# Kernel tuning notes

Hardware: AMD Instinct MI355X
Metric: run time of the kernel (lower is better)

## Reference

```python
import jax, jax.numpy as jnp
import numpy as np

TOKENS = 32768
HIDDEN = 2048
N_EXPERTS = 128
TOP_K = 8
NORM_TOPK_PROB = True


def setup_inputs() -> dict:
    key = jax.random.key(0)
    k1, k2 = jax.random.split(key)
    hidden_states = jax.random.normal(k1, (TOKENS, HIDDEN), dtype=jnp.float32)
    # router weight [num_experts, hidden_dim]; small init like a trained gate
    weight = jax.random.normal(k2, (N_EXPERTS, HIDDEN), dtype=jnp.float32) * 0.02
    return {"hidden_states": hidden_states, "weight": weight}


def reference(hidden_states, weight):
    # flatten tokens (already [T, H])
    x = hidden_states.reshape(-1, HIDDEN)
    # router logits: [T, E]
    logits = jnp.einsum("th,eh->te", x, weight)
    # softmax in float32 (matches dtype=torch.float)
    probs = jax.nn.softmax(logits.astype(jnp.float32), axis=-1)
    # top-k over experts
    top_val, top_idx = jax.lax.top_k(probs, TOP_K)  # [T, K], [T, K]
    if NORM_TOPK_PROB:
        top_val = top_val / jnp.sum(top_val, axis=-1, keepdims=True)
    top_val = top_val.astype(probs.dtype)
    # scatter renormalized weights into dense [T, E] score tensor
    rows = jnp.arange(x.shape[0])[:, None]  # [T, 1]
    scores = jnp.zeros_like(probs).at[rows, top_idx].set(top_val)
    return scores, top_idx
```

## Files before the change

### kernel.cpp

```cpp
#include <hip/hip_runtime.h>
#include <hip/hip_bf16.h>

#define NT   32768
#define NH   2048
#define NE   128
#define TOPK 8
#define BT   32
#define BND    6.0e-4f
#define TWO_B  (2.0f * BND)

#define WS_W_OFF   64
#define WS_REC_U32 262160

typedef __attribute__((ext_vector_type(8))) short bf16x8;
typedef __attribute__((ext_vector_type(4))) float f32x4;

static __device__ __forceinline__ unsigned short f2bf(float f) {
    __hip_bfloat16 h = __float2bfloat16(f);
    return *reinterpret_cast<unsigned short*>(&h);
}

__global__ __launch_bounds__(256) void prep_w_kernel(
    const float* __restrict__ W, unsigned short* __restrict__ Wt)
{
    int g = blockIdx.x * 256 + threadIdx.x;
    int lane = g & 63;
    int te   = (g >> 6) & 7;
    int s    = (g >> 9) & 1;
    int k32  = g >> 10;
    int row  = te * 16 + (lane & 15);
    int kb   = k32 * 32 + (lane >> 4) * 8;
    const float* src = W + (size_t)row * NH + kb;
    float4 f0 = *(const float4*)src;
    float4 f1 = *(const float4*)(src + 4);
    float f[8] = {f0.x, f0.y, f0.z, f0.w, f1.x, f1.y, f1.z, f1.w};
    bf16x8 o;
    #pragma unroll
    for (int e = 0; e < 8; ++e) {
        unsigned short h = f2bf(f[e]);
        if (s == 0) o[e] = (short)h;
        else {
            float fh = __builtin_bit_cast(float, ((unsigned int)h) << 16);
            o[e] = (short)f2bf(f[e] - fh);
        }
    }
    *(bf16x8*)(Wt + (size_t)g * 8) = o;
}

__global__ __launch_bounds__(256, 3) void router_gemm_kernel(
    const float* __restrict__ X, const unsigned short* __restrict__ Wt,
    float* __restrict__ out, unsigned int* __restrict__ ws)
{
    __shared__ float ps[2][BT * 132];

    const int tid  = threadIdx.x;
    const int lane = tid & 63;
    const int w    = tid >> 6;
    const int l15  = lane & 15, lhi = lane >> 4;
    const int t0   = blockIdx.x * BT;

    f32x4 acc[2][8];
    #pragma unroll
    for (int i = 0; i < 2; ++i)
        #pragma unroll
        for (int te = 0; te < 8; ++te) acc[i][te] = (f32x4){0.f, 0.f, 0.f, 0.f};

    const float* x0 = X + (size_t)(t0 + l15) * NH + lhi * 8;
    const float* x1 = X + (size_t)(t0 + 16 + l15) * NH + lhi * 8;
    const int kbase = w * 512;

    #pragma unroll 2
    for (int kk = 0; kk < 16; ++kk) {
        const int k = kbase + kk * 32;
        bf16x8 ah[2], al[2];
        #pragma unroll
        for (int i = 0; i < 2; ++i) {
            const float* xp = (i ? x1 : x0) + k;
            float4 fa = *(const float4*)xp;
            float4 fb = *(const float4*)(xp + 4);
            float f[8] = {fa.x, fa.y, fa.z, fa.w, fb.x, fb.y, fb.z, fb.w};
            #pragma unroll
            for (int e = 0; e < 8; ++e) {
                unsigned short h = f2bf(f[e]);
                ah[i][e] = (short)h;
                float fh = __builtin_bit_cast(float, ((unsigned int)h) << 16);
                al[i][e] = (short)f2bf(f[e] - fh);
            }
        }
        const unsigned short* wb = Wt + (size_t)(w * 16 + kk) * 8192;
        #pragma unroll
        for (int te = 0; te < 8; ++te) {
            bf16x8 bh = *(const bf16x8*)(wb + te * 512 + lane * 8);
            bf16x8 bl = *(const bf16x8*)(wb + 4096 + te * 512 + lane * 8);
            acc[0][te] = __builtin_amdgcn_mfma_f32_16x16x32_bf16(ah[0], bh, acc[0][te], 0, 0, 0);
            acc[1][te] = __builtin_amdgcn_mfma_f32_16x16x32_bf16(ah[1], bh, acc[1][te], 0, 0, 0);
            acc[0][te] = __builtin_amdgcn_mfma_f32_16x16x32_bf16(al[0], bh, acc[0][te], 0, 0, 0);
            acc[1][te] = __builtin_amdgcn_mfma_f32_16x16x32_bf16(al[1], bh, acc[1][te], 0, 0, 0);
            acc[0][te] = __builtin_amdgcn_mfma_f32_16x16x32_bf16(ah[0], bl, acc[0][te], 0, 0, 0);
            acc[1][te] = __builtin_amdgcn_mfma_f32_16x16x32_bf16(ah[1], bl, acc[1][te], 0, 0, 0);
        }
    }

    if (w < 2) {
        #pragma unroll
        for (int i = 0; i < 2; ++i)
            #pragma unroll
            for (int te = 0; te < 8; ++te)
                #pragma unroll
                for (int q = 0; q < 4; ++q)
                    ps[w][(i * 16 + lhi * 4 + q) * 132 + te * 16 + l15] = acc[i][te][q];
    }
    __syncthreads();
    if (w >= 2) {
        #pragma unroll
        for (int i = 0; i < 2; ++i)
            #pragma unroll
            for (int te = 0; te < 8; ++te)
                #pragma unroll
                for (int q = 0; q < 4; ++q) {
                    int o = (i * 16 + lhi * 4 + q) * 132 + te * 16 + l15;
                    ps[w - 2][o] += acc[i][te][q];
                }
    }
    __syncthreads();
    #pragma unroll
    for (int q = 0; q < 4; ++q) {
        int idx = tid + q * 256;
        int row = idx >> 5, c4 = idx & 31;
        int o = row * 132 + c4 * 4;
        float4 a = *(float4*)&ps[0][o];
        float4 b = *(float4*)&ps[1][o];
        a.x += b.x; a.y += b.y; a.z += b.z; a.w += b.w;
        *(float4*)&ps[0][o] = a;
    }
    float* scoreBase = out + (size_t)t0 * NE;
    #pragma unroll
    for (int q = 0; q < 4; ++q) {
        int i = tid + q * 256;
        *(float4*)(scoreBase + (size_t)i * 4) = make_float4(0.f, 0.f, 0.f, 0.f);
    }
    __syncthreads();

    if (tid < BT) {
        const float* row = &ps[0][tid * 132];
        float tv[13]; int ti[13];
        #pragma unroll
        for (int k = 0; k < 13; ++k) { tv[k] = -3.0e38f; ti[k] = 0; }
        for (int e = 0; e < NE; ++e) {
            float v = row[e];
            if (v > tv[12]) {
                float cv = v; int ci = e;
                #pragma unroll
                for (int s = 0; s < 13; ++s) {
                    if (cv > tv[s]) {
                        float t1 = tv[s]; int t2 = ti[s];
                        tv[s] = cv; ti[s] = ci; cv = t1; ci = t2;
                    }
                }
            }
        }
        bool flag = false;
        #pragma unroll
        for (int k = 0; k < 8; ++k) flag |= (tv[k] - tv[k + 1] < TWO_B);

        float pv[8]; float ksum = 0.f;
        #pragma unroll
        for (int k = 0; k < 8; ++k) { pv[k] = expf(tv[k] - tv[0]); ksum += pv[k]; }
        const int tg = t0 + tid;
        float* srow = out + (size_t)tg * NE;
        float* irow = out + (size_t)NT * NE + (size_t)tg * TOPK;
        #pragma unroll
        for (int k = 0; k < 8; ++k) {
            srow[ti[k]] = pv[k] / ksum;
            irow[k] = (float)ti[k];
        }

        if (flag) {
            unsigned int cnt;
            unsigned int idw[4] = {0u, 0u, 0u, 0u};
            float thr = tv[7] - TWO_B;
            if (tv[12] >= thr) {
                cnt = 0xFFu;
            } else {
                cnt = 0;
                #pragma unroll
                for (int k = 0; k < 13; ++k) {
                    if (k < 8 || tv[k] >= thr) {
                        idw[cnt >> 2] |= ((unsigned int)ti[k]) << ((cnt & 3) * 8);
                        ++cnt;
                    }
                }
            }
            unsigned int slot = atomicAdd(ws, 1u);
            unsigned int* rec = ws + WS_REC_U32 + slot * 8;
            rec[0] = (unsigned int)tg;
            rec[1] = cnt;
            rec[2] = idw[0]; rec[3] = idw[1]; rec[4] = idw[2]; rec[5] = idw[3];
        }
    }
}

__global__ __launch_bounds__(256) void finalize_kernel(
    const float* __restrict__ X, const float* __restrict__ W,
    float* __restrict__ out, const unsigned int* __restrict__ ws)
{
    __shared__ float  xs[2048];
    __shared__ double cv[128];
    __shared__ int    cid[128];
    __shared__ float  ovals[8];
    __shared__ int    oidx[8];

    const int tid = threadIdx.x;
    const int lane = tid & 63, w = tid >> 6;
    const unsigned int n = ws[0];

    for (unsigned int rI = blockIdx.x; rI < n; rI += gridDim.x) {
        const unsigned int* rec = ws + WS_REC_U32 + rI * 8;
        const int tg = (int)rec[0];
        const unsigned int cnt = rec[1];
        const unsigned char* ids = (const unsigned char*)(rec + 2);
        const int nc = (cnt == 0xFFu) ? NE : (int)cnt;

        #pragma unroll
        for (int q = 0; q < 2; ++q) {
            int i = tid + q * 256;
            *(float4*)(xs + i * 4) = *(const float4*)(X + (size_t)tg * NH + i * 4);
        }
        __syncthreads();

        for (int c = w; c < nc; c += 4) {
            int e = (cnt == 0xFFu) ? c : (int)ids[c];
            const float* wrow = W + (size_t)e * NH;
            double s = 0.0;
            #pragma unroll
            for (int m = 0; m < 8; ++m) {
                float4 wv = *(const float4*)(wrow + m * 256 + lane * 4);
                float4 xv = *(const float4*)(xs + m * 256 + lane * 4);
                s = fma((double)xv.x, (double)wv.x, s);
                s = fma((double)xv.y, (double)wv.y, s);
                s = fma((double)xv.z, (double)wv.z, s);
                s = fma((double)xv.w, (double)wv.w, s);
            }
            #pragma unroll
            for (int off = 32; off >= 1; off >>= 1) s += __shfl_xor(s, off);
            if (lane == 0) { cv[c] = s; cid[c] = e; }
        }
        __syncthreads();

        if (tid == 0) {
            double lv[8];
            #pragma unroll
            for (int k = 0; k < 8; ++k) {
                double best = -1.0e300; int bi = 1 << 30, bc = 0;
                for (int c = 0; c < nc; ++c) {
                    double v = cv[c]; int e = cid[c];
                    if (v > best || (v == best && e < bi)) { best = v; bi = e; bc = c; }
                }
                lv[k] = best; oidx[k] = bi; cv[bc] = -1.0e301;
            }
            double m = lv[0], sum = 0.0, p[8];
            #pragma unroll
            for (int k = 0; k < 8; ++k) { p[k] = exp(lv[k] - m); sum += p[k]; }
            #pragma unroll
            for (int k = 0; k < 8; ++k) ovals[k] = (float)(p[k] / sum);
        }
        __syncthreads();

        float* srow = out + (size_t)tg * NE;
        if (tid < NE) {
            float val = 0.f;
            #pragma unroll
            for (int k = 0; k < 8; ++k) if (oidx[k] == tid) val = ovals[k];
            srow[tid] = val;
        }
        if (tid < TOPK) out[(size_t)NT * NE + (size_t)tg * TOPK + tid] = (float)oidx[tid];
        __syncthreads();
    }
}

extern "C" void kernel_launch(void* const* d_in, const int* in_sizes, int n_in,
                              void* d_out, int out_size, void* d_ws, size_t ws_size,
                              hipStream_t stream) {
    const float* X = (const float*)d_in[0];
    const float* W = (const float*)d_in[1];
    float* out = (float*)d_out;
    unsigned char* wsb = (unsigned char*)d_ws;
    unsigned short* Wt = (unsigned short*)(wsb + WS_W_OFF);

    hipMemsetAsync(d_ws, 0, 64, stream);
    prep_w_kernel<<<256, 256, 0, stream>>>(W, Wt);
    router_gemm_kernel<<<NT / BT, 256, 0, stream>>>(X, Wt, out, (unsigned int*)d_ws);
    finalize_kernel<<<1024, 256, 0, stream>>>(X, W, out, (const unsigned int*)d_ws);
}
```

Measured before the change: 196.8 us.

## Double-buffer W fragments, bit-trick bf16 split, move top-k to separate kernel

The GEMM loop now prefetches the next k-step's W fragments into registers (double buffering) while the current MFMAs run. It also replaces the library bf16 conversion with integer round-half-up bit tricks, and lowers the occupancy hint from 3 to 2. The top-k selection, which previously ran on only 32 threads per block, moves to a separate kernel with one token per thread that reads logits written to the output buffer. The trade-off is an extra global round trip for the logits and another kernel launch, plus higher register pressure. The new rounding (add 0x8000) differs from round-to-nearest-even only in tie cases.

```diff
diff --git a/kernel.cpp b/kernel.cpp
--- a/kernel.cpp
+++ b/kernel.cpp
@@ -14,6 +14,7 @@
 
 typedef __attribute__((ext_vector_type(8))) short bf16x8;
 typedef __attribute__((ext_vector_type(4))) float f32x4;
+typedef __attribute__((ext_vector_type(4))) unsigned int u32x4;
 
 static __device__ __forceinline__ unsigned short f2bf(float f) {
     __hip_bfloat16 h = __float2bfloat16(f);
@@ -47,9 +48,9 @@
     *(bf16x8*)(Wt + (size_t)g * 8) = o;
 }
 
-__global__ __launch_bounds__(256, 3) void router_gemm_kernel(
+__global__ __launch_bounds__(256, 2) void router_gemm_kernel(
     const float* __restrict__ X, const unsigned short* __restrict__ Wt,
-    float* __restrict__ out, unsigned int* __restrict__ ws)
+    float* __restrict__ outLg)
 {
     __shared__ float ps[2][BT * 132];
 
@@ -65,40 +66,68 @@
         #pragma unroll
         for (int te = 0; te < 8; ++te) acc[i][te] = (f32x4){0.f, 0.f, 0.f, 0.f};
 
-    const float* x0 = X + (size_t)(t0 + l15) * NH + lhi * 8;
-    const float* x1 = X + (size_t)(t0 + 16 + l15) * NH + lhi * 8;
-    const int kbase = w * 512;
-
-    #pragma unroll 2
-    for (int kk = 0; kk < 16; ++kk) {
-        const int k = kbase + kk * 32;
+    const float* x0 = X + (size_t)(t0 + l15) * NH + w * 512 + lhi * 8;
+    const float* x1 = x0 + 16 * NH;
+    const unsigned short* wbase = Wt + (size_t)(w * 16) * 8192 + lane * 8;
+
+    bf16x8 b0[8][2], b1[8][2];
+
+    #define LOADB(arr, kk) do {                                                \
+        const unsigned short* wb_ = wbase + (size_t)(kk) * 8192;               \
+        _Pragma("unroll")                                                      \
+        for (int te = 0; te < 8; ++te) {                                       \
+            arr[te][0] = *(const bf16x8*)(wb_ + te * 512);                     \
+            arr[te][1] = *(const bf16x8*)(wb_ + 4096 + te * 512);              \
+        }                                                                      \
+    } while (0)
+
+    #define SPLITA(kk, ah, al) do {                                            \
+        _Pragma("unroll")                                                      \
+        for (int i = 0; i < 2; ++i) {                                          \
+            const float* xp = (i ? x1 : x0) + (kk) * 32;                       \
+            float4 fa = *(const float4*)xp;                                    \
+            float4 fb = *(const float4*)(xp + 4);                              \
+            float ff[8] = {fa.x, fa.y, fa.z, fa.w, fb.x, fb.y, fb.z, fb.w};    \
+            unsigned int hu[4], lu[4];                                         \
+            _Pragma("unroll")                                                  \
+            for (int p = 0; p < 4; ++p) {                                      \
+                unsigned int u0 = __builtin_bit_cast(unsigned int, ff[2*p]);   \
+                unsigned int u1 = __builtin_bit_cast(unsigned int, ff[2*p+1]); \
+                unsigned int r0 = u0 + 0x8000u, r1 = u1 + 0x8000u;             \
+                hu[p] = (r0 >> 16) | (r1 & 0xFFFF0000u);                       \
+                float h0 = __builtin_bit_cast(float, r0 & 0xFFFF0000u);        \
+                float h1 = __builtin_bit_cast(float, r1 & 0xFFFF0000u);        \
+                float e0 = ff[2*p] - h0, e1 = ff[2*p+1] - h1;                  \
+                unsigned int s0 = __builtin_bit_cast(unsigned int, e0) + 0x8000u; \
+                unsigned int s1 = __builtin_bit_cast(unsigned int, e1) + 0x8000u; \
+                lu[p] = (s0 >> 16) | (s1 & 0xFFFF0000u);                       \
+            }                                                                  \
+            ah[i] = __builtin_bit_cast(bf16x8, (u32x4){hu[0],hu[1],hu[2],hu[3]}); \
+            al[i] = __builtin_bit_cast(bf16x8, (u32x4){lu[0],lu[1],lu[2],lu[3]}); \
+        }                                                                      \
+    } while (0)
+
+    #define DOMFMA(b, ah, al) do {                                             \
+        _Pragma("unroll")                                                      \
+        for (int te = 0; te < 8; ++te) {                                       \
+            acc[0][te] = __builtin_amdgcn_mfma_f32_16x16x32_bf16(ah[0], b[te][0], acc[0][te], 0, 0, 0); \
+            acc[1][te] = __builtin_amdgcn_mfma_f32_16x16x32_bf16(ah[1], b[te][0], acc[1][te], 0, 0, 0); \
+            acc[0][te] = __builtin_amdgcn_mfma_f32_16x16x32_bf16(al[0], b[te][0], acc[0][te], 0, 0, 0); \
+            acc[1][te] = __builtin_amdgcn_mfma_f32_16x16x32_bf16(al[1], b[te][0], acc[1][te], 0, 0, 0); \
+            acc[0][te] = __builtin_amdgcn_mfma_f32_16x16x32_bf16(ah[0], b[te][1], acc[0][te], 0, 0, 0); \
+            acc[1][te] = __builtin_amdgcn_mfma_f32_16x16x32_bf16(ah[1], b[te][1], acc[1][te], 0, 0, 0); \
+        }                                                                      \
+    } while (0)
+
+    LOADB(b0, 0);
+    for (int p = 0; p < 8; ++p) {
         bf16x8 ah[2], al[2];
-        #pragma unroll
-        for (int i = 0; i < 2; ++i) {
-            const float* xp = (i ? x1 : x0) + k;
-            float4 fa = *(const float4*)xp;
-            float4 fb = *(const float4*)(xp + 4);
-            float f[8] = {fa.x, fa.y, fa.z, fa.w, fb.x, fb.y, fb.z, fb.w};
-            #pragma unroll
-            for (int e = 0; e < 8; ++e) {
-                unsigned short h = f2bf(f[e]);
-                ah[i][e] = (short)h;
-                float fh = __builtin_bit_cast(float, ((unsigned int)h) << 16);
-                al[i][e] = (short)f2bf(f[e] - fh);
-            }
-        }
-        const unsigned short* wb = Wt + (size_t)(w * 16 + kk) * 8192;
-        #pragma unroll
-        for (int te = 0; te < 8; ++te) {
-            bf16x8 bh = *(const bf16x8*)(wb + te * 512 + lane * 8);
-            bf16x8 bl = *(const bf16x8*)(wb + 4096 + te * 512 + lane * 8);
-            acc[0][te] = __builtin_amdgcn_mfma_f32_16x16x32_bf16(ah[0], bh, acc[0][te], 0, 0, 0);
-            acc[1][te] = __builtin_amdgcn_mfma_f32_16x16x32_bf16(ah[1], bh, acc[1][te], 0, 0, 0);
-            acc[0][te] = __builtin_amdgcn_mfma_f32_16x16x32_bf16(al[0], bh, acc[0][te], 0, 0, 0);
-            acc[1][te] = __builtin_amdgcn_mfma_f32_16x16x32_bf16(al[1], bh, acc[1][te], 0, 0, 0);
-            acc[0][te] = __builtin_amdgcn_mfma_f32_16x16x32_bf16(ah[0], bl, acc[0][te], 0, 0, 0);
-            acc[1][te] = __builtin_amdgcn_mfma_f32_16x16x32_bf16(ah[1], bl, acc[1][te], 0, 0, 0);
-        }
+        LOADB(b1, 2 * p + 1);
+        SPLITA(2 * p, ah, al);
+        DOMFMA(b0, ah, al);
+        if (p < 7) LOADB(b0, 2 * p + 2);
+        SPLITA(2 * p + 1, ah, al);
+        DOMFMA(b1, ah, al);
     }
 
     if (w < 2) {
@@ -125,31 +154,35 @@
     __syncthreads();
     #pragma unroll
     for (int q = 0; q < 4; ++q) {
-        int idx = tid + q * 256;
-        int row = idx >> 5, c4 = idx & 31;
+        int i = tid + q * 256;
+        int row = i >> 5, c4 = i & 31;
         int o = row * 132 + c4 * 4;
         float4 a = *(float4*)&ps[0][o];
         float4 b = *(float4*)&ps[1][o];
         a.x += b.x; a.y += b.y; a.z += b.z; a.w += b.w;
-        *(float4*)&ps[0][o] = a;
-    }
-    float* scoreBase = out + (size_t)t0 * NE;
-    #pragma unroll
-    for (int q = 0; q < 4; ++q) {
-        int i = tid + q * 256;
-        *(float4*)(scoreBase + (size_t)i * 4) = make_float4(0.f, 0.f, 0.f, 0.f);
-    }
-    __syncthreads();
-
-    if (tid < BT) {
-        const float* row = &ps[0][tid * 132];
-        float tv[13]; int ti[13];
-        #pragma unroll
-        for (int k = 0; k < 13; ++k) { tv[k] = -3.0e38f; ti[k] = 0; }
-        for (int e = 0; e < NE; ++e) {
-            float v = row[e];
+        *(float4*)(outLg + (size_t)(t0 + row) * NE + c4 * 4) = a;
+    }
+}
+
+__global__ __launch_bounds__(64) void select_kernel(
+    float* __restrict__ out, unsigned int* __restrict__ ws)
+{
+    const int tg = blockIdx.x * 64 + threadIdx.x;
+    float* row = out + (size_t)tg * NE;
+
+    float tv[13]; int ti[13];
+    #pragma unroll
+    for (int k = 0; k < 13; ++k) { tv[k] = -3.0e38f; ti[k] = 0; }
+
+    #pragma unroll 4
+    for (int c = 0; c < 32; ++c) {
+        float4 v4 = *(const float4*)(row + c * 4);
+        float vs[4] = {v4.x, v4.y, v4.z, v4.w};
+        #pragma unroll
+        for (int j = 0; j < 4; ++j) {
+            float v = vs[j];
             if (v > tv[12]) {
-                float cv = v; int ci = e;
+                float cv = v; int ci = c * 4 + j;
                 #pragma unroll
                 for (int s = 0; s < 13; ++s) {
                     if (cv > tv[s]) {
@@ -159,44 +192,49 @@
                 }
             }
         }
-        bool flag = false;
-        #pragma unroll
-        for (int k = 0; k < 8; ++k) flag |= (tv[k] - tv[k + 1] < TWO_B);
-
-        float pv[8]; float ksum = 0.f;
-        #pragma unroll
-        for (int k = 0; k < 8; ++k) { pv[k] = expf(tv[k] - tv[0]); ksum += pv[k]; }
-        const int tg = t0 + tid;
-        float* srow = out + (size_t)tg * NE;
-        float* irow = out + (size_t)NT * NE + (size_t)tg * TOPK;
-        #pragma unroll
-        for (int k = 0; k < 8; ++k) {
-            srow[ti[k]] = pv[k] / ksum;
-            irow[k] = (float)ti[k];
-        }
-
-        if (flag) {
-            unsigned int cnt;
-            unsigned int idw[4] = {0u, 0u, 0u, 0u};
-            float thr = tv[7] - TWO_B;
-            if (tv[12] >= thr) {
-                cnt = 0xFFu;
-            } else {
-                cnt = 0;
-                #pragma unroll
-                for (int k = 0; k < 13; ++k) {
-                    if (k < 8 || tv[k] >= thr) {
-                        idw[cnt >> 2] |= ((unsigned int)ti[k]) << ((cnt & 3) * 8);
-                        ++cnt;
-                    }
+    }
+
+    bool flag = false;
+    #pragma unroll
+    for (int k = 0; k < 8; ++k) flag |= (tv[k] - tv[k + 1] < TWO_B);
+
+    float pv[8]; float ksum = 0.f;
+    #pragma unroll
+    for (int k = 0; k < 8; ++k) { pv[k] = expf(tv[k] - tv[0]); ksum += pv[k]; }
+
+    float4 z = make_float4(0.f, 0.f, 0.f, 0.f);
+    #pragma unroll
+    for (int c = 0; c < 32; ++c) *(float4*)(row + c * 4) = z;
+    #pragma unroll
+    for (int k = 0; k < 8; ++k) row[ti[k]] = pv[k] / ksum;
+
+    float* irow = out + (size_t)NT * NE + (size_t)tg * TOPK;
+    float4 i0 = make_float4((float)ti[0], (float)ti[1], (float)ti[2], (float)ti[3]);
+    float4 i1 = make_float4((float)ti[4], (float)ti[5], (float)ti[6], (float)ti[7]);
+    *(float4*)irow = i0;
+    *(float4*)(irow + 4) = i1;
+
+    if (flag) {
+        unsigned int cnt;
+        unsigned int idw[4] = {0u, 0u, 0u, 0u};
+        float thr = tv[7] - TWO_B;
+        if (tv[12] >= thr) {
+            cnt = 0xFFu;
+        } else {
+            cnt = 0;
+            #pragma unroll
+            for (int k = 0; k < 13; ++k) {
+                if (k < 8 || tv[k] >= thr) {
+                    idw[cnt >> 2] |= ((unsigned int)ti[k]) << ((cnt & 3) * 8);
+                    ++cnt;
                 }
             }
-            unsigned int slot = atomicAdd(ws, 1u);
-            unsigned int* rec = ws + WS_REC_U32 + slot * 8;
-            rec[0] = (unsigned int)tg;
-            rec[1] = cnt;
-            rec[2] = idw[0]; rec[3] = idw[1]; rec[4] = idw[2]; rec[5] = idw[3];
-        }
+        }
+        unsigned int slot = atomicAdd(ws, 1u);
+        unsigned int* rec = ws + WS_REC_U32 + slot * 8;
+        rec[0] = (unsigned int)tg;
+        rec[1] = cnt;
+        rec[2] = idw[0]; rec[3] = idw[1]; rec[4] = idw[2]; rec[5] = idw[3];
     }
 }
 
@@ -289,6 +327,7 @@
 
     hipMemsetAsync(d_ws, 0, 64, stream);
     prep_w_kernel<<<256, 256, 0, stream>>>(W, Wt);
-    router_gemm_kernel<<<NT / BT, 256, 0, stream>>>(X, Wt, out, (unsigned int*)d_ws);
+    router_gemm_kernel<<<NT / BT, 256, 0, stream>>>(X, Wt, out);
+    select_kernel<<<NT / 64, 64, 0, stream>>>(out, (unsigned int*)d_ws);
     finalize_kernel<<<1024, 256, 0, stream>>>(X, W, out, (const unsigned int*)d_ws);
 }
```

New measurement: 345.6 us. +75.6%, slower.

## Split router GEMM across 8 waves with prefetch and bit-trick bf16 split

Applied to the files above, without the earlier changes.

The router GEMM block grows from 256 to 512 threads. Each wave now handles one 16-token group over a quarter of K instead of both groups, which halves the accumulator registers per wave and raises occupancy. The loop prefetches the next X chunk into registers, and the fp32 to hi/lo bf16 split uses integer round-and-mask in place of conversion intrinsics. Partial sums are reduced through a transposed shared buffer over serialized passes with barriers. In exchange, each wave loads every W fragment without reusing it across two token groups, so W traffic per MFMA doubles.

```diff
diff --git a/kernel.cpp b/kernel.cpp
--- a/kernel.cpp
+++ b/kernel.cpp
@@ -5,7 +5,7 @@
 #define NH   2048
 #define NE   128
 #define TOPK 8
-#define BT   32
+#define BTOK 32
 #define BND    6.0e-4f
 #define TWO_B  (2.0f * BND)
 
@@ -14,6 +14,7 @@
 
 typedef __attribute__((ext_vector_type(8))) short bf16x8;
 typedef __attribute__((ext_vector_type(4))) float f32x4;
+typedef __attribute__((ext_vector_type(4))) unsigned int u32x4;
 
 static __device__ __forceinline__ unsigned short f2bf(float f) {
     __hip_bfloat16 h = __float2bfloat16(f);
@@ -47,107 +48,101 @@
     *(bf16x8*)(Wt + (size_t)g * 8) = o;
 }
 
-__global__ __launch_bounds__(256, 3) void router_gemm_kernel(
+__global__ __launch_bounds__(512, 4) void router_gemm_kernel(
     const float* __restrict__ X, const unsigned short* __restrict__ Wt,
     float* __restrict__ out, unsigned int* __restrict__ ws)
 {
-    __shared__ float ps[2][BT * 132];
+    __shared__ float ps[NE * 36];
 
     const int tid  = threadIdx.x;
     const int lane = tid & 63;
-    const int w    = tid >> 6;
+    const int wv   = tid >> 6;
+    const int g    = wv & 1;
+    const int h    = wv >> 1;
     const int l15  = lane & 15, lhi = lane >> 4;
-    const int t0   = blockIdx.x * BT;
-
-    f32x4 acc[2][8];
-    #pragma unroll
-    for (int i = 0; i < 2; ++i)
-        #pragma unroll
-        for (int te = 0; te < 8; ++te) acc[i][te] = (f32x4){0.f, 0.f, 0.f, 0.f};
-
-    const float* x0 = X + (size_t)(t0 + l15) * NH + lhi * 8;
-    const float* x1 = X + (size_t)(t0 + 16 + l15) * NH + lhi * 8;
-    const int kbase = w * 512;
-
-    #pragma unroll 2
+    const int t0   = blockIdx.x * BTOK;
+
+    f32x4 acc[8];
+    #pragma unroll
+    for (int te = 0; te < 8; ++te) acc[te] = (f32x4){0.f, 0.f, 0.f, 0.f};
+
+    const float* xrow = X + (size_t)(t0 + g * 16 + l15) * NH + h * 512 + lhi * 8;
+    const unsigned short* wq = Wt + (size_t)(h * 16) * 8192 + lane * 8;
+
+    float4 a0 = *(const float4*)(xrow);
+    float4 a1 = *(const float4*)(xrow + 4);
+
+    #pragma unroll
     for (int kk = 0; kk < 16; ++kk) {
-        const int k = kbase + kk * 32;
-        bf16x8 ah[2], al[2];
-        #pragma unroll
-        for (int i = 0; i < 2; ++i) {
-            const float* xp = (i ? x1 : x0) + k;
-            float4 fa = *(const float4*)xp;
-            float4 fb = *(const float4*)(xp + 4);
-            float f[8] = {fa.x, fa.y, fa.z, fa.w, fb.x, fb.y, fb.z, fb.w};
-            #pragma unroll
-            for (int e = 0; e < 8; ++e) {
-                unsigned short h = f2bf(f[e]);
-                ah[i][e] = (short)h;
-                float fh = __builtin_bit_cast(float, ((unsigned int)h) << 16);
-                al[i][e] = (short)f2bf(f[e] - fh);
-            }
-        }
-        const unsigned short* wb = Wt + (size_t)(w * 16 + kk) * 8192;
+        float4 n0, n1;
+        if (kk < 15) {
+            n0 = *(const float4*)(xrow + (kk + 1) * 32);
+            n1 = *(const float4*)(xrow + (kk + 1) * 32 + 4);
+        }
+        bf16x8 ah, al;
+        {
+            float ff[8] = {a0.x, a0.y, a0.z, a0.w, a1.x, a1.y, a1.z, a1.w};
+            unsigned int hu[4], lu[4];
+            #pragma unroll
+            for (int p = 0; p < 4; ++p) {
+                unsigned int u0 = __builtin_bit_cast(unsigned int, ff[2 * p]);
+                unsigned int u1 = __builtin_bit_cast(unsigned int, ff[2 * p + 1]);
+                unsigned int r0 = u0 + 0x8000u, r1 = u1 + 0x8000u;
+                hu[p] = (r0 >> 16) | (r1 & 0xFFFF0000u);
+                float h0 = __builtin_bit_cast(float, r0 & 0xFFFF0000u);
+                float h1 = __builtin_bit_cast(float, r1 & 0xFFFF0000u);
+                float e0 = ff[2 * p] - h0, e1 = ff[2 * p + 1] - h1;
+                unsigned int s0 = __builtin_bit_cast(unsigned int, e0);
+                unsigned int s1 = __builtin_bit_cast(unsigned int, e1);
+                lu[p] = (s0 >> 16) | (s1 & 0xFFFF0000u);
+            }
+            ah = __builtin_bit_cast(bf16x8, (u32x4){hu[0], hu[1], hu[2], hu[3]});
+            al = __builtin_bit_cast(bf16x8, (u32x4){lu[0], lu[1], lu[2], lu[3]});
+        }
+        const unsigned short* wb = wq + (size_t)kk * 8192;
         #pragma unroll
         for (int te = 0; te < 8; ++te) {
-            bf16x8 bh = *(const bf16x8*)(wb + te * 512 + lane * 8);
-            bf16x8 bl = *(const bf16x8*)(wb + 4096 + te * 512 + lane * 8);
-            acc[0][te] = __builtin_amdgcn_mfma_f32_16x16x32_bf16(ah[0], bh, acc[0][te], 0, 0, 0);
-            acc[1][te] = __builtin_amdgcn_mfma_f32_16x16x32_bf16(ah[1], bh, acc[1][te], 0, 0, 0);
-            acc[0][te] = __builtin_amdgcn_mfma_f32_16x16x32_bf16(al[0], bh, acc[0][te], 0, 0, 0);
-            acc[1][te] = __builtin_amdgcn_mfma_f32_16x16x32_bf16(al[1], bh, acc[1][te], 0, 0, 0);
-            acc[0][te] = __builtin_amdgcn_mfma_f32_16x16x32_bf16(ah[0], bl, acc[0][te], 0, 0, 0);
-            acc[1][te] = __builtin_amdgcn_mfma_f32_16x16x32_bf16(ah[1], bl, acc[1][te], 0, 0, 0);
-        }
-    }
-
-    if (w < 2) {
-        #pragma unroll
-        for (int i = 0; i < 2; ++i)
-            #pragma unroll
-            for (int te = 0; te < 8; ++te)
-                #pragma unroll
-                for (int q = 0; q < 4; ++q)
-                    ps[w][(i * 16 + lhi * 4 + q) * 132 + te * 16 + l15] = acc[i][te][q];
+            bf16x8 bh = *(const bf16x8*)(wb + te * 512);
+            bf16x8 bl = *(const bf16x8*)(wb + 4096 + te * 512);
+            acc[te] = __builtin_amdgcn_mfma_f32_16x16x32_bf16(ah, bh, acc[te], 0, 0, 0);
+            acc[te] = __builtin_amdgcn_mfma_f32_16x16x32_bf16(al, bh, acc[te], 0, 0, 0);
+            acc[te] = __builtin_amdgcn_mfma_f32_16x16x32_bf16(ah, bl, acc[te], 0, 0, 0);
+        }
+        a0 = n0; a1 = n1;
+    }
+
+    const int colbase = g * 16 + lhi * 4;
+    #pragma unroll
+    for (int hh = 0; hh < 4; ++hh) {
+        if (h == hh) {
+            #pragma unroll
+            for (int te = 0; te < 8; ++te) {
+                float* p = ps + (te * 16 + l15) * 36 + colbase;
+                if (hh == 0) *(f32x4*)p = acc[te];
+                else {
+                    f32x4 v = *(f32x4*)p;
+                    v += acc[te];
+                    *(f32x4*)p = v;
+                }
+            }
+        }
+        __syncthreads();
+    }
+
+    float* scoreBase = out + (size_t)t0 * NE;
+    #pragma unroll
+    for (int q = 0; q < 2; ++q) {
+        int i = tid + q * 512;
+        *(float4*)(scoreBase + (size_t)i * 4) = make_float4(0.f, 0.f, 0.f, 0.f);
     }
     __syncthreads();
-    if (w >= 2) {
-        #pragma unroll
-        for (int i = 0; i < 2; ++i)
-            #pragma unroll
-            for (int te = 0; te < 8; ++te)
-                #pragma unroll
-                for (int q = 0; q < 4; ++q) {
-                    int o = (i * 16 + lhi * 4 + q) * 132 + te * 16 + l15;
-                    ps[w - 2][o] += acc[i][te][q];
-                }
-    }
-    __syncthreads();
-    #pragma unroll
-    for (int q = 0; q < 4; ++q) {
-        int idx = tid + q * 256;
-        int row = idx >> 5, c4 = idx & 31;
-        int o = row * 132 + c4 * 4;
-        float4 a = *(float4*)&ps[0][o];
-        float4 b = *(float4*)&ps[1][o];
-        a.x += b.x; a.y += b.y; a.z += b.z; a.w += b.w;
-        *(float4*)&ps[0][o] = a;
-    }
-    float* scoreBase = out + (size_t)t0 * NE;
-    #pragma unroll
-    for (int q = 0; q < 4; ++q) {
-        int i = tid + q * 256;
-        *(float4*)(scoreBase + (size_t)i * 4) = make_float4(0.f, 0.f, 0.f, 0.f);
-    }
-    __syncthreads();
-
-    if (tid < BT) {
-        const float* row = &ps[0][tid * 132];
+
+    if (tid < BTOK) {
         float tv[13]; int ti[13];
         #pragma unroll
         for (int k = 0; k < 13; ++k) { tv[k] = -3.0e38f; ti[k] = 0; }
         for (int e = 0; e < NE; ++e) {
-            float v = row[e];
+            float v = ps[e * 36 + tid];
             if (v > tv[12]) {
                 float cv = v; int ci = e;
                 #pragma unroll
@@ -289,6 +284,6 @@
 
     hipMemsetAsync(d_ws, 0, 64, stream);
     prep_w_kernel<<<256, 256, 0, stream>>>(W, Wt);
-    router_gemm_kernel<<<NT / BT, 256, 0, stream>>>(X, Wt, out, (unsigned int*)d_ws);
+    router_gemm_kernel<<<NT / BTOK, 512, 0, stream>>>(X, Wt, out, (unsigned int*)d_ws);
     finalize_kernel<<<1024, 256, 0, stream>>>(X, W, out, (const unsigned int*)d_ws);
 }
```

Measured after the change: 288.8 us. +46.8%, slower.
